# Kernel tuning notes

Measured on AMD Instinct MI355X. Metric: run time of the kernel, lower is better.

The kernel has to match this reference:

```python
import jax, jax.numpy as jnp
import numpy as np

N = 2_000_000
F = 32  # feature_num
GH = GW = 256


def _bilinear_interpolate(grid, coords):
    # grid: [H, W, F], coords: [N, 2] in (0,1)
    W = grid.shape[1] - 1
    H = grid.shape[0] - 1
    x = coords[:, 0] * W
    y = coords[:, 1] * H
    x0 = x.astype(jnp.int32)
    y0 = y.astype(jnp.int32)
    xf = x % 1
    yf = y % 1
    x1 = jnp.minimum(x0 + 1, W)
    y1 = jnp.minimum(y0 + 1, H)
    tl = grid[y0, x0]  # [N, F]
    tr = grid[y0, x1]
    bl = grid[y1, x0]
    br = grid[y1, x1]
    top = (1 - xf)[:, None] * tl + xf[:, None] * tr
    bot = (1 - xf)[:, None] * bl + xf[:, None] * br
    return (1 - yf)[:, None] * top + yf[:, None] * bot


def setup_inputs() -> dict:
    key = jax.random.key(0)
    ks = jax.random.split(key, 16)
    inp = {
        "pos": jax.random.uniform(ks[0], (N, 2), dtype=jnp.float32),
        "dir": jax.random.uniform(ks[1], (N, 2), dtype=jnp.float32),
        # grids: randn * 10 as in the torch module
        "pos_grid": jax.random.normal(ks[2], (GH, GW, F), dtype=jnp.float32) * 10.0,
        "dir_grid": jax.random.normal(ks[3], (GH, GW, F), dtype=jnp.float32) * 10.0,
        # shared encoder: Linear(2,4), Linear(4,3)
        "enc_w1": jax.random.normal(ks[4], (2, 4), dtype=jnp.float32) * 0.5,
        "enc_b1": jax.random.normal(ks[5], (4,), dtype=jnp.float32) * 0.1,
        "enc_w2": jax.random.normal(ks[6], (4, 3), dtype=jnp.float32) * 0.5,
        "enc_b2": jax.random.normal(ks[7], (3,), dtype=jnp.float32) * 0.1,
        # fc head: 2F -> 64 -> 16 -> 8 -> 3
        "fc_w1": jax.random.normal(ks[8], (2 * F, 64), dtype=jnp.float32) * 0.1,
        "fc_b1": jnp.zeros((64,), dtype=jnp.float32),
        "fc_w2": jax.random.normal(ks[9], (64, 16), dtype=jnp.float32) * 0.1,
        "fc_b2": jnp.zeros((16,), dtype=jnp.float32),
        "fc_w3": jax.random.normal(ks[10], (16, 8), dtype=jnp.float32) * 0.1,
        "fc_b3": jnp.zeros((8,), dtype=jnp.float32),
        "fc_w4": jax.random.normal(ks[11], (8, 3), dtype=jnp.float32) * 0.1,
        "fc_b4": jnp.zeros((3,), dtype=jnp.float32),
    }
    return inp


def reference(pos, dir, pos_grid, dir_grid,
              enc_w1, enc_b1, enc_w2, enc_b2,
              fc_w1, fc_b1, fc_w2, fc_b2, fc_w3, fc_b3, fc_w4, fc_b4):
    def encoder(x):
        h = jnp.tanh(x @ enc_w1 + enc_b1)
        return jax.nn.sigmoid(h @ enc_w2 + enc_b2)  # [N, 3]; only cols 0,1 used

    p = encoder(pos)
    d = encoder(dir)
    # features are .detach()'ed in the original
    pos_feat = jax.lax.stop_gradient(_bilinear_interpolate(pos_grid, p))
    dir_feat = jax.lax.stop_gradient(_bilinear_interpolate(dir_grid, d))
    x = jnp.concatenate([pos_feat, dir_feat], axis=1)  # [N, 2F]
    # Dropout layers are identity in eval mode
    x = jax.nn.leaky_relu(x @ fc_w1 + fc_b1)
    x = jax.nn.leaky_relu(x @ fc_w2 + fc_b2)
    x = jax.nn.leaky_relu(x @ fc_w3 + fc_b3)
    x = jax.nn.leaky_relu(x @ fc_w4 + fc_b4)
    return jax.nn.sigmoid(x) * 255.0
```

## Files before the change

kernel.cpp:

```cpp
#include <hip/hip_runtime.h>
#include <math.h>

typedef __attribute__((ext_vector_type(8))) __bf16 bf16x8;
typedef __attribute__((ext_vector_type(4))) __bf16 bf16x4;
typedef __attribute__((ext_vector_type(4))) float floatx4;
typedef __attribute__((ext_vector_type(8))) float floatx8;

__device__ __forceinline__ float fast_rcp(float x) { return __builtin_amdgcn_rcpf(x); }
__device__ __forceinline__ float sigmoidf_(float z) { return fast_rcp(1.0f + __expf(-z)); }
__device__ __forceinline__ float fast_tanh(float z) {
    float e = __expf(2.0f * z);
    return 1.0f - 2.0f * fast_rcp(e + 1.0f);
}
__device__ __forceinline__ float leaky(float v) { return fmaxf(v, 0.01f * v); }

__device__ __forceinline__ int swzb(int row, int byteoff) {
    return row * 128 + (byteoff ^ ((row & 7) << 4));
}

__device__ __forceinline__ void gload_lds16(const __bf16* g, char* l) {
    __builtin_amdgcn_global_load_lds((const __attribute__((address_space(1))) void*)g,
                                     (__attribute__((address_space(3))) void*)l, 16, 0, 0);
}

__global__ void convert_grids(const float* __restrict__ g0, const float* __restrict__ g1,
                              __bf16* __restrict__ o0, __bf16* __restrict__ o1, int elems) {
    int i = blockIdx.x * blockDim.x + threadIdx.x;
    int nvec = elems >> 2;
    if (i < nvec) {
        float4 v = ((const float4*)g0)[i];
        bf16x4 r = { (__bf16)v.x, (__bf16)v.y, (__bf16)v.z, (__bf16)v.w };
        ((bf16x4*)o0)[i] = r;
    } else if (i < 2 * nvec) {
        int j = i - nvec;
        float4 v = ((const float4*)g1)[j];
        bf16x4 r = { (__bf16)v.x, (__bf16)v.y, (__bf16)v.z, (__bf16)v.w };
        ((bf16x4*)o1)[j] = r;
    }
}

template<bool BF16G>
__global__ __launch_bounds__(256, 2) void gridnet_fwd(
    const float2* __restrict__ pos, const float2* __restrict__ dir_,
    const float* __restrict__ pos_gridf, const float* __restrict__ dir_gridf,
    const __bf16* __restrict__ pos_gridb, const __bf16* __restrict__ dir_gridb,
    const float* __restrict__ enc_w1, const float* __restrict__ enc_b1,
    const float* __restrict__ enc_w2, const float* __restrict__ enc_b2,
    const float* __restrict__ fc_w1, const float* __restrict__ fc_b1,
    const float* __restrict__ fc_w2, const float* __restrict__ fc_b2,
    const float* __restrict__ fc_w3, const float* __restrict__ fc_b3,
    const float* __restrict__ fc_w4, const float* __restrict__ fc_b4,
    float* __restrict__ out, int n)
{
    __shared__ __align__(1024) char smem[32768 + 32768 + 8192 + 2048];
    __shared__ float b1lds[64];
    __shared__ float b2lds[16];

    const int tid  = threadIdx.x;
    const int lane = tid & 63;
    const int wid  = tid >> 6;
    const int quad = lane >> 4;
    const int l15  = lane & 15;

    char* Xw  = smem + wid * 8192;
    char* Stg = smem + 32768 + wid * 8192;
    char* W1p = smem + 65536;
    char* W2p = smem + 65536 + 8192;

    for (int idx = tid; idx < 4096; idx += 256)
        *(__bf16*)(W1p + swzb(idx & 63, (idx >> 6) * 2)) = (__bf16)fc_w1[idx];
    for (int idx = tid; idx < 1024; idx += 256)
        *(__bf16*)(W2p + swzb(idx & 15, (idx >> 4) * 2)) = (__bf16)fc_w2[idx];
    if (tid < 64) b1lds[tid] = fc_b1[tid];
    if (tid < 16) b2lds[tid] = fc_b2[tid];
    __syncthreads();

    int i  = blockIdx.x * 256 + wid * 64 + lane;
    int ic = min(i, n - 1);

    unsigned pcp[2];
    float xfp[2], yfp[2];
    #pragma unroll
    for (int pass = 0; pass < 2; ++pass) {
        float2 xy = pass ? dir_[ic] : pos[ic];
        float hh[4];
        #pragma unroll
        for (int k = 0; k < 4; ++k)
            hh[k] = fast_tanh(xy.x * enc_w1[k] + xy.y * enc_w1[4 + k] + enc_b1[k]);
        float e0 = enc_b2[0], e1 = enc_b2[1];
        #pragma unroll
        for (int k = 0; k < 4; ++k) {
            e0 += hh[k] * enc_w2[3 * k + 0];
            e1 += hh[k] * enc_w2[3 * k + 1];
        }
        float x = sigmoidf_(e0) * 255.0f;
        float y = sigmoidf_(e1) * 255.0f;
        int x0 = (int)x, y0 = (int)y;
        xfp[pass] = x - (float)x0;
        yfp[pass] = y - (float)y0;
        int x1 = min(x0 + 1, 255), y1 = min(y0 + 1, 255);
        pcp[pass] = (unsigned)x0 | ((unsigned)y0 << 8) | ((unsigned)x1 << 16) | ((unsigned)y1 << 24);
    }

    if (BF16G) {
        const int m3 = lane & 3;
        const int ck = (lane >> 2) & 3;
        const int cc = lane >> 4;
        const int bq = lane >> 2;
        const int bk = lane & 3;

        {
            #pragma unroll
            for (int j = 0; j < 4; ++j) {
                unsigned pcq = (unsigned)__shfl((int)pcp[0], j * 4 + m3);
                int xq = (cc & 1) ? ((pcq >> 16) & 255) : (pcq & 255);
                int yq = (cc & 2) ? (int)(pcq >> 24) : (int)((pcq >> 8) & 255);
                gload_lds16(pos_gridb + ((yq << 8) + xq) * 32 + ck * 8, Stg + j * 1024);
            }
        }

        #pragma unroll
        for (int it = 0; it < 8; ++it) {
            const int pass = it >> 2, j16 = it & 3;
            const int buf = (it & 1) * 4096;
            if (it < 7) {
                const int nit = it + 1, np = nit >> 2, nj16 = nit & 3;
                const __bf16* g = np ? dir_gridb : pos_gridb;
                #pragma unroll
                for (int j = 0; j < 4; ++j) {
                    unsigned pcq = (unsigned)__shfl((int)pcp[np], nj16 * 16 + j * 4 + m3);
                    int xq = (cc & 1) ? ((pcq >> 16) & 255) : (pcq & 255);
                    int yq = (cc & 2) ? (int)(pcq >> 24) : (int)((pcq >> 8) & 255);
                    gload_lds16(g + ((yq << 8) + xq) * 32 + ck * 8,
                                Stg + ((nit & 1) * 4096) + j * 1024);
                }
            }
            float xfq = __shfl(xfp[pass], j16 * 16 + bq);
            float yfq = __shfl(yfp[pass], j16 * 16 + bq);
            float oxf = 1.0f - xfq, oyf = 1.0f - yfq;
            float w0 = oyf * oxf, w1 = oyf * xfq, w2 = yfq * oxf, w3 = yfq * xfq;

            if (it < 7) __asm__ volatile("s_waitcnt vmcnt(4)" ::: "memory");
            else        __asm__ volatile("s_waitcnt vmcnt(0)" ::: "memory");

            const char* sb = Stg + buf + (lane >> 4) * 1024 + bk * 64 + ((lane >> 2) & 3) * 16;
            bf16x8 c0 = *(const bf16x8*)(sb + 0);
            bf16x8 c1 = *(const bf16x8*)(sb + 256);
            bf16x8 c2 = *(const bf16x8*)(sb + 512);
            bf16x8 c3 = *(const bf16x8*)(sb + 768);
            floatx8 r = w0 * __builtin_convertvector(c0, floatx8)
                      + w1 * __builtin_convertvector(c1, floatx8)
                      + w2 * __builtin_convertvector(c2, floatx8)
                      + w3 * __builtin_convertvector(c3, floatx8);
            int q = j16 * 16 + bq;
            *(bf16x8*)(Xw + swzb(q, pass * 64 + bk * 16)) = __builtin_convertvector(r, bf16x8);
        }
    } else {
        #pragma unroll
        for (int pass = 0; pass < 2; ++pass) {
            const float* g = pass ? dir_gridf : pos_gridf;
            unsigned pcq = pcp[pass];
            int x0 = pcq & 255, y0 = (pcq >> 8) & 255, x1 = (pcq >> 16) & 255, y1 = pcq >> 24;
            float xfq = xfp[pass], yfq = yfp[pass];
            float oxf = 1.0f - xfq, oyf = 1.0f - yfq;
            float w0 = oyf * oxf, w1 = oyf * xfq, w2 = yfq * oxf, w3 = yfq * xfq;
            int ctl = ((y0 << 8) + x0) << 5, ctr = ((y0 << 8) + x1) << 5;
            int cbl = ((y1 << 8) + x0) << 5, cbr = ((y1 << 8) + x1) << 5;
            #pragma unroll
            for (int c = 0; c < 4; ++c) {
                floatx8 fa = *(const floatx8*)(g + ctl + c * 8);
                floatx8 fb = *(const floatx8*)(g + ctr + c * 8);
                floatx8 fc = *(const floatx8*)(g + cbl + c * 8);
                floatx8 fd = *(const floatx8*)(g + cbr + c * 8);
                floatx8 r = w0 * fa + w1 * fb + w2 * fc + w3 * fd;
                *(bf16x8*)(Xw + swzb(lane, pass * 64 + c * 16)) = __builtin_convertvector(r, bf16x8);
            }
        }
    }

    __asm__ volatile("s_waitcnt lgkmcnt(0)" ::: "memory");

    bf16x8 wf[2][4];
    #pragma unroll
    for (int ks = 0; ks < 2; ++ks)
        #pragma unroll
        for (int mt = 0; mt < 4; ++mt)
            wf[ks][mt] = *(const bf16x8*)(W1p + swzb(mt * 16 + l15, ks * 64 + quad * 16));

    floatx4 b1v[4];
    #pragma unroll
    for (int mt = 0; mt < 4; ++mt)
        b1v[mt] = *(const floatx4*)(b1lds + mt * 16 + quad * 4);

    floatx4 acc[4][4];
    #pragma unroll
    for (int mt = 0; mt < 4; ++mt)
        #pragma unroll
        for (int nt = 0; nt < 4; ++nt)
            acc[mt][nt] = b1v[mt];

    #pragma unroll
    for (int ks = 0; ks < 2; ++ks) {
        bf16x8 xf[4];
        #pragma unroll
        for (int nt = 0; nt < 4; ++nt)
            xf[nt] = *(const bf16x8*)(Xw + swzb(nt * 16 + l15, ks * 64 + quad * 16));
        #pragma unroll
        for (int mt = 0; mt < 4; ++mt)
            #pragma unroll
            for (int nt = 0; nt < 4; ++nt)
                acc[mt][nt] = __builtin_amdgcn_mfma_f32_16x16x32_bf16(wf[ks][mt], xf[nt], acc[mt][nt], 0, 0, 0);
    }

    #pragma unroll
    for (int mt = 0; mt < 4; ++mt)
        #pragma unroll
        for (int nt = 0; nt < 4; ++nt) {
            bf16x4 hv;
            #pragma unroll
            for (int r = 0; r < 4; ++r)
                hv[r] = (__bf16)leaky(acc[mt][nt][r]);
            *(bf16x4*)(Xw + swzb(nt * 16 + l15, mt * 32 + quad * 8)) = hv;
        }
    __asm__ volatile("s_waitcnt lgkmcnt(0)" ::: "memory");

    bf16x8 w2f[2];
    #pragma unroll
    for (int ks = 0; ks < 2; ++ks)
        w2f[ks] = *(const bf16x8*)(W2p + swzb(l15, ks * 64 + quad * 16));
    floatx4 b2v = *(const floatx4*)(b2lds + quad * 4);
    floatx4 acc2[4];
    #pragma unroll
    for (int nt = 0; nt < 4; ++nt) acc2[nt] = b2v;
    #pragma unroll
    for (int ks = 0; ks < 2; ++ks) {
        #pragma unroll
        for (int nt = 0; nt < 4; ++nt) {
            bf16x8 hf = *(const bf16x8*)(Xw + swzb(nt * 16 + l15, ks * 64 + quad * 16));
            acc2[nt] = __builtin_amdgcn_mfma_f32_16x16x32_bf16(w2f[ks], hf, acc2[nt], 0, 0, 0);
        }
    }

    #pragma unroll
    for (int nt = 0; nt < 4; ++nt) {
        floatx4 hv;
        #pragma unroll
        for (int r = 0; r < 4; ++r)
            hv[r] = leaky(acc2[nt][r]);
        *(floatx4*)(Xw + swzb(nt * 16 + l15, quad * 16)) = hv;
    }
    __asm__ volatile("s_waitcnt lgkmcnt(0)" ::: "memory");

    float h2[16];
    #pragma unroll
    for (int c = 0; c < 4; ++c) {
        floatx4 v = *(const floatx4*)(Xw + swzb(lane, c * 16));
        h2[4 * c + 0] = v[0]; h2[4 * c + 1] = v[1]; h2[4 * c + 2] = v[2]; h2[4 * c + 3] = v[3];
    }
    float h3[8];
    #pragma unroll
    for (int j = 0; j < 8; ++j) h3[j] = fc_b3[j];
    #pragma unroll
    for (int k = 0; k < 16; ++k) {
        float xv = h2[k];
        #pragma unroll
        for (int j = 0; j < 8; ++j) h3[j] = fmaf(xv, fc_w3[(k << 3) + j], h3[j]);
    }
    #pragma unroll
    for (int j = 0; j < 8; ++j) h3[j] = leaky(h3[j]);

    float o[3];
    #pragma unroll
    for (int j = 0; j < 3; ++j) o[j] = fc_b4[j];
    #pragma unroll
    for (int k = 0; k < 8; ++k) {
        float xv = h3[k];
        #pragma unroll
        for (int j = 0; j < 3; ++j) o[j] = fmaf(xv, fc_w4[3 * k + j], o[j]);
    }
    if (i < n) {
        #pragma unroll
        for (int j = 0; j < 3; ++j)
            out[3 * i + j] = sigmoidf_(leaky(o[j])) * 255.0f;
    }
}

extern "C" void kernel_launch(void* const* d_in, const int* in_sizes, int n_in,
                              void* d_out, int out_size, void* d_ws, size_t ws_size,
                              hipStream_t stream) {
    int n = in_sizes[0] / 2;
    const int GELEMS = 256 * 256 * 32;
    bool use_bf16 = ws_size >= (size_t)(2 * GELEMS * sizeof(__bf16));
    __bf16* g0 = (__bf16*)d_ws;
    __bf16* g1 = g0 + GELEMS;

    if (use_bf16) {
        int total = 2 * (GELEMS / 4);
        convert_grids<<<(total + 255) / 256, 256, 0, stream>>>(
            (const float*)d_in[2], (const float*)d_in[3], g0, g1, GELEMS);
    }

    int blocks = (n + 255) / 256;
    if (use_bf16) {
        gridnet_fwd<true><<<blocks, 256, 0, stream>>>(
            (const float2*)d_in[0], (const float2*)d_in[1],
            (const float*)d_in[2], (const float*)d_in[3], g0, g1,
            (const float*)d_in[4], (const float*)d_in[5],
            (const float*)d_in[6], (const float*)d_in[7],
            (const float*)d_in[8], (const float*)d_in[9],
            (const float*)d_in[10], (const float*)d_in[11],
            (const float*)d_in[12], (const float*)d_in[13],
            (const float*)d_in[14], (const float*)d_in[15],
            (float*)d_out, n);
    } else {
        gridnet_fwd<false><<<blocks, 256, 0, stream>>>(
            (const float2*)d_in[0], (const float2*)d_in[1],
            (const float*)d_in[2], (const float*)d_in[3], g0, g1,
            (const float*)d_in[4], (const float*)d_in[5],
            (const float*)d_in[6], (const float*)d_in[7],
            (const float*)d_in[8], (const float*)d_in[9],
            (const float*)d_in[10], (const float*)d_in[11],
            (const float*)d_in[12], (const float*)d_in[13],
            (const float*)d_in[14], (const float*)d_in[15],
            (float*)d_out, n);
    }
}
```

Before: 255.6 us.

## Gather bilinear corners directly into MFMA B-fragment registers, drop LDS staging

Replaces the double-buffered global_load_lds staging pipeline with direct per-lane global loads. Each lane fetches the 8-channel slice of the four corners it needs for the MFMA B operand, interpolates in registers and feeds the result straight into the first-layer MFMA, skipping the LDS round trip. This frees 32KB of staging LDS per block, so launch bounds go from 2 to 3 blocks per CU. The cost is that the hand-scheduled vmcnt prefetch overlap is gone and latency hiding now depends on occupancy and compiler scheduling. Register pressure also rises from holding the 8 gathered fragments.

```diff
diff --git a/kernel.cpp b/kernel.cpp
--- a/kernel.cpp
+++ b/kernel.cpp
@@ -16,11 +16,6 @@
 
 __device__ __forceinline__ int swzb(int row, int byteoff) {
     return row * 128 + (byteoff ^ ((row & 7) << 4));
-}
-
-__device__ __forceinline__ void gload_lds16(const __bf16* g, char* l) {
-    __builtin_amdgcn_global_load_lds((const __attribute__((address_space(1))) void*)g,
-                                     (__attribute__((address_space(3))) void*)l, 16, 0, 0);
 }
 
 __global__ void convert_grids(const float* __restrict__ g0, const float* __restrict__ g1,
@@ -40,7 +35,7 @@
 }
 
 template<bool BF16G>
-__global__ __launch_bounds__(256, 2) void gridnet_fwd(
+__global__ __launch_bounds__(256, 3) void gridnet_fwd(
     const float2* __restrict__ pos, const float2* __restrict__ dir_,
     const float* __restrict__ pos_gridf, const float* __restrict__ dir_gridf,
     const __bf16* __restrict__ pos_gridb, const __bf16* __restrict__ dir_gridb,
@@ -52,7 +47,7 @@
     const float* __restrict__ fc_w4, const float* __restrict__ fc_b4,
     float* __restrict__ out, int n)
 {
-    __shared__ __align__(1024) char smem[32768 + 32768 + 8192 + 2048];
+    __shared__ __align__(1024) char smem[32768 + 8192 + 2048];
     __shared__ float b1lds[64];
     __shared__ float b2lds[16];
 
@@ -62,10 +57,9 @@
     const int quad = lane >> 4;
     const int l15  = lane & 15;
 
-    char* Xw  = smem + wid * 8192;
-    char* Stg = smem + 32768 + wid * 8192;
-    char* W1p = smem + 65536;
-    char* W2p = smem + 65536 + 8192;
+    char* Hw  = smem + wid * 8192;
+    char* W1p = smem + 32768;
+    char* W2p = smem + 32768 + 8192;
 
     for (int idx = tid; idx < 4096; idx += 256)
         *(__bf16*)(W1p + swzb(idx & 63, (idx >> 6) * 2)) = (__bf16)fc_w1[idx];
@@ -75,6 +69,17 @@
     if (tid < 16) b2lds[tid] = fc_b2[tid];
     __syncthreads();
 
+    bf16x8 wf[2][4];
+    #pragma unroll
+    for (int ks = 0; ks < 2; ++ks)
+        #pragma unroll
+        for (int mt = 0; mt < 4; ++mt)
+            wf[ks][mt] = *(const bf16x8*)(W1p + swzb(mt * 16 + l15, ks * 64 + quad * 16));
+    floatx4 b1v[4];
+    #pragma unroll
+    for (int mt = 0; mt < 4; ++mt)
+        b1v[mt] = *(const floatx4*)(b1lds + mt * 16 + quad * 4);
+
     int i  = blockIdx.x * 256 + wid * 64 + lane;
     int ic = min(i, n - 1);
 
@@ -102,95 +107,40 @@
         pcp[pass] = (unsigned)x0 | ((unsigned)y0 << 8) | ((unsigned)x1 << 16) | ((unsigned)y1 << 24);
     }
 
-    if (BF16G) {
-        const int m3 = lane & 3;
-        const int ck = (lane >> 2) & 3;
-        const int cc = lane >> 4;
-        const int bq = lane >> 2;
-        const int bk = lane & 3;
-
-        {
-            #pragma unroll
-            for (int j = 0; j < 4; ++j) {
-                unsigned pcq = (unsigned)__shfl((int)pcp[0], j * 4 + m3);
-                int xq = (cc & 1) ? ((pcq >> 16) & 255) : (pcq & 255);
-                int yq = (cc & 2) ? (int)(pcq >> 24) : (int)((pcq >> 8) & 255);
-                gload_lds16(pos_gridb + ((yq << 8) + xq) * 32 + ck * 8, Stg + j * 1024);
+    bf16x8 xfr[2][4];
+    #pragma unroll
+    for (int ks = 0; ks < 2; ++ks) {
+        #pragma unroll
+        for (int nt = 0; nt < 4; ++nt) {
+            const int src = nt * 16 + l15;
+            unsigned pcq = (unsigned)__shfl((int)pcp[ks], src);
+            float xfq = __shfl(xfp[ks], src);
+            float yfq = __shfl(yfp[ks], src);
+            int x0 = pcq & 255, y0 = (pcq >> 8) & 255;
+            int x1 = (pcq >> 16) & 255, y1 = pcq >> 24;
+            float oxf = 1.0f - xfq, oyf = 1.0f - yfq;
+            floatx8 r;
+            if (BF16G) {
+                const __bf16* ga = (ks ? dir_gridb : pos_gridb) + quad * 8;
+                bf16x8 va = *(const bf16x8*)(ga + (((y0 << 8) + x0) << 5));
+                bf16x8 vb = *(const bf16x8*)(ga + (((y0 << 8) + x1) << 5));
+                bf16x8 vc = *(const bf16x8*)(ga + (((y1 << 8) + x0) << 5));
+                bf16x8 vd = *(const bf16x8*)(ga + (((y1 << 8) + x1) << 5));
+                r = (oyf * oxf) * __builtin_convertvector(va, floatx8)
+                  + (oyf * xfq) * __builtin_convertvector(vb, floatx8)
+                  + (yfq * oxf) * __builtin_convertvector(vc, floatx8)
+                  + (yfq * xfq) * __builtin_convertvector(vd, floatx8);
+            } else {
+                const float* ga = (ks ? dir_gridf : pos_gridf) + quad * 8;
+                floatx8 va = *(const floatx8*)(ga + (((y0 << 8) + x0) << 5));
+                floatx8 vb = *(const floatx8*)(ga + (((y0 << 8) + x1) << 5));
+                floatx8 vc = *(const floatx8*)(ga + (((y1 << 8) + x0) << 5));
+                floatx8 vd = *(const floatx8*)(ga + (((y1 << 8) + x1) << 5));
+                r = (oyf * oxf) * va + (oyf * xfq) * vb + (yfq * oxf) * vc + (yfq * xfq) * vd;
             }
-        }
-
-        #pragma unroll
-        for (int it = 0; it < 8; ++it) {
-            const int pass = it >> 2, j16 = it & 3;
-            const int buf = (it & 1) * 4096;
-            if (it < 7) {
-                const int nit = it + 1, np = nit >> 2, nj16 = nit & 3;
-                const __bf16* g = np ? dir_gridb : pos_gridb;
-                #pragma unroll
-                for (int j = 0; j < 4; ++j) {
-                    unsigned pcq = (unsigned)__shfl((int)pcp[np], nj16 * 16 + j * 4 + m3);
-                    int xq = (cc & 1) ? ((pcq >> 16) & 255) : (pcq & 255);
-                    int yq = (cc & 2) ? (int)(pcq >> 24) : (int)((pcq >> 8) & 255);
-                    gload_lds16(g + ((yq << 8) + xq) * 32 + ck * 8,
-                                Stg + ((nit & 1) * 4096) + j * 1024);
-                }
-            }
-            float xfq = __shfl(xfp[pass], j16 * 16 + bq);
-            float yfq = __shfl(yfp[pass], j16 * 16 + bq);
-            float oxf = 1.0f - xfq, oyf = 1.0f - yfq;
-            float w0 = oyf * oxf, w1 = oyf * xfq, w2 = yfq * oxf, w3 = yfq * xfq;
-
-            if (it < 7) __asm__ volatile("s_waitcnt vmcnt(4)" ::: "memory");
-            else        __asm__ volatile("s_waitcnt vmcnt(0)" ::: "memory");
-
-            const char* sb = Stg + buf + (lane >> 4) * 1024 + bk * 64 + ((lane >> 2) & 3) * 16;
-            bf16x8 c0 = *(const bf16x8*)(sb + 0);
-            bf16x8 c1 = *(const bf16x8*)(sb + 256);
-            bf16x8 c2 = *(const bf16x8*)(sb + 512);
-            bf16x8 c3 = *(const bf16x8*)(sb + 768);
-            floatx8 r = w0 * __builtin_convertvector(c0, floatx8)
-                      + w1 * __builtin_convertvector(c1, floatx8)
-                      + w2 * __builtin_convertvector(c2, floatx8)
-                      + w3 * __builtin_convertvector(c3, floatx8);
-            int q = j16 * 16 + bq;
-            *(bf16x8*)(Xw + swzb(q, pass * 64 + bk * 16)) = __builtin_convertvector(r, bf16x8);
-        }
-    } else {
-        #pragma unroll
-        for (int pass = 0; pass < 2; ++pass) {
-            const float* g = pass ? dir_gridf : pos_gridf;
-            unsigned pcq = pcp[pass];
-            int x0 = pcq & 255, y0 = (pcq >> 8) & 255, x1 = (pcq >> 16) & 255, y1 = pcq >> 24;
-            float xfq = xfp[pass], yfq = yfp[pass];
-            float oxf = 1.0f - xfq, oyf = 1.0f - yfq;
-            float w0 = oyf * oxf, w1 = oyf * xfq, w2 = yfq * oxf, w3 = yfq * xfq;
-            int ctl = ((y0 << 8) + x0) << 5, ctr = ((y0 << 8) + x1) << 5;
-            int cbl = ((y1 << 8) + x0) << 5, cbr = ((y1 << 8) + x1) << 5;
-            #pragma unroll
-            for (int c = 0; c < 4; ++c) {
-                floatx8 fa = *(const floatx8*)(g + ctl + c * 8);
-                floatx8 fb = *(const floatx8*)(g + ctr + c * 8);
-                floatx8 fc = *(const floatx8*)(g + cbl + c * 8);
-                floatx8 fd = *(const floatx8*)(g + cbr + c * 8);
-                floatx8 r = w0 * fa + w1 * fb + w2 * fc + w3 * fd;
-                *(bf16x8*)(Xw + swzb(lane, pass * 64 + c * 16)) = __builtin_convertvector(r, bf16x8);
-            }
-        }
-    }
-
-    __asm__ volatile("s_waitcnt lgkmcnt(0)" ::: "memory");
-
-    bf16x8 wf[2][4];
-    #pragma unroll
-    for (int ks = 0; ks < 2; ++ks)
-        #pragma unroll
-        for (int mt = 0; mt < 4; ++mt)
-            wf[ks][mt] = *(const bf16x8*)(W1p + swzb(mt * 16 + l15, ks * 64 + quad * 16));
-
-    floatx4 b1v[4];
-    #pragma unroll
-    for (int mt = 0; mt < 4; ++mt)
-        b1v[mt] = *(const floatx4*)(b1lds + mt * 16 + quad * 4);
+            xfr[ks][nt] = __builtin_convertvector(r, bf16x8);
+        }
+    }
 
     floatx4 acc[4][4];
     #pragma unroll
@@ -198,19 +148,13 @@
         #pragma unroll
         for (int nt = 0; nt < 4; ++nt)
             acc[mt][nt] = b1v[mt];
-
-    #pragma unroll
-    for (int ks = 0; ks < 2; ++ks) {
-        bf16x8 xf[4];
-        #pragma unroll
-        for (int nt = 0; nt < 4; ++nt)
-            xf[nt] = *(const bf16x8*)(Xw + swzb(nt * 16 + l15, ks * 64 + quad * 16));
+    #pragma unroll
+    for (int ks = 0; ks < 2; ++ks)
         #pragma unroll
         for (int mt = 0; mt < 4; ++mt)
             #pragma unroll
             for (int nt = 0; nt < 4; ++nt)
-                acc[mt][nt] = __builtin_amdgcn_mfma_f32_16x16x32_bf16(wf[ks][mt], xf[nt], acc[mt][nt], 0, 0, 0);
-    }
+                acc[mt][nt] = __builtin_amdgcn_mfma_f32_16x16x32_bf16(wf[ks][mt], xfr[ks][nt], acc[mt][nt], 0, 0, 0);
 
     #pragma unroll
     for (int mt = 0; mt < 4; ++mt)
@@ -220,7 +164,7 @@
             #pragma unroll
             for (int r = 0; r < 4; ++r)
                 hv[r] = (__bf16)leaky(acc[mt][nt][r]);
-            *(bf16x4*)(Xw + swzb(nt * 16 + l15, mt * 32 + quad * 8)) = hv;
+            *(bf16x4*)(Hw + swzb(nt * 16 + l15, mt * 32 + quad * 8)) = hv;
         }
     __asm__ volatile("s_waitcnt lgkmcnt(0)" ::: "memory");
 
@@ -236,7 +180,7 @@
     for (int ks = 0; ks < 2; ++ks) {
         #pragma unroll
         for (int nt = 0; nt < 4; ++nt) {
-            bf16x8 hf = *(const bf16x8*)(Xw + swzb(nt * 16 + l15, ks * 64 + quad * 16));
+            bf16x8 hf = *(const bf16x8*)(Hw + swzb(nt * 16 + l15, ks * 64 + quad * 16));
             acc2[nt] = __builtin_amdgcn_mfma_f32_16x16x32_bf16(w2f[ks], hf, acc2[nt], 0, 0, 0);
         }
     }
@@ -247,14 +191,14 @@
         #pragma unroll
         for (int r = 0; r < 4; ++r)
             hv[r] = leaky(acc2[nt][r]);
-        *(floatx4*)(Xw + swzb(nt * 16 + l15, quad * 16)) = hv;
+        *(floatx4*)(Hw + swzb(nt * 16 + l15, quad * 16)) = hv;
     }
     __asm__ volatile("s_waitcnt lgkmcnt(0)" ::: "memory");
 
     float h2[16];
     #pragma unroll
     for (int c = 0; c < 4; ++c) {
-        floatx4 v = *(const floatx4*)(Xw + swzb(lane, c * 16));
+        floatx4 v = *(const floatx4*)(Hw + swzb(lane, c * 16));
         h2[4 * c + 0] = v[0]; h2[4 * c + 1] = v[1]; h2[4 * c + 2] = v[2]; h2[4 * c + 3] = v[3];
     }
     float h3[8];
```

After: 218.0 us. 1.17x faster.
